# Kernel tuning notes

Hardware: AMD Instinct MI355X
Metric: run time of the kernel (lower is better)

The kernel has to match this reference:

```python
import jax, jax.numpy as jnp
import numpy as np

EPS = 1e-5

def conv_bn(x, w, bn):
    # 1x1 conv (no bias) + BatchNorm2d in eval mode.
    # x: [B,C,H,W], w: [O,C], bn: [4,O] = (gamma, beta, running_mean, running_var)
    y = jnp.einsum('bchw,oc->bohw', x, w)
    g, b, m, v = bn[0], bn[1], bn[2], bn[3]
    s = g * jax.lax.rsqrt(v + EPS)
    return y * s[None, :, None, None] + (b - m * s)[None, :, None, None]

def setup_inputs() -> dict:
    key = jax.random.key(0)
    ks = jax.random.split(key, 10)
    dim, nh_kd, dh = 384, 256, 1024
    return {
        'x':   jax.random.normal(ks[0], (16, dim, 32, 32), dtype=jnp.float32),
        'wq':  jax.random.normal(ks[1], (nh_kd, dim), dtype=jnp.float32) * 0.05,
        'bnq': jax.random.uniform(ks[2], (4, nh_kd), dtype=jnp.float32),
        'wk':  jax.random.normal(ks[3], (nh_kd, dim), dtype=jnp.float32) * 0.05,
        'bnk': jax.random.uniform(ks[4], (4, nh_kd), dtype=jnp.float32),
        'wv':  jax.random.normal(ks[5], (dh, dim), dtype=jnp.float32) * 0.05,
        'bnv': jax.random.uniform(ks[6], (4, dh), dtype=jnp.float32),
        'wp':  jax.random.normal(ks[7], (dim, dh), dtype=jnp.float32) * 0.05,
        'bnp': jax.random.uniform(ks[8], (4, dim), dtype=jnp.float32),
        'num_heads': 8,
    }

def reference(x, wq, bnq, wk, bnk, wv, bnv, wp, bnp, num_heads):
    B, C, H, W = x.shape
    N = H * W
    nh = num_heads
    kd = wq.shape[0] // nh          # key_dim
    d = wv.shape[0] // nh           # attn_ratio * key_dim
    dh = wv.shape[0]
    scale = kd ** (-0.5)

    qq = conv_bn(x, wq, bnq).reshape(B, nh, kd, N).transpose(0, 1, 3, 2)  # [B,nh,N,kd]
    kk = conv_bn(x, wk, bnk).reshape(B, nh, kd, N)                         # [B,nh,kd,N]
    vv = conv_bn(x, wv, bnv).reshape(B, nh, d, N).transpose(0, 1, 3, 2)    # [B,nh,N,d]

    # NOTE: original divides by scale (i.e. multiplies by sqrt(key_dim)); kept faithfully.
    attn = jnp.einsum('bhnk,bhkm->bhnm', qq, kk) / scale
    attn = jax.nn.softmax(attn, axis=-1)
    xx = jnp.einsum('bhnm,bhmd->bhnd', attn, vv)           # [B,nh,N,d]
    xx = xx.transpose(0, 1, 3, 2).reshape(B, dh, H, W)
    return conv_bn(xx, wp, bnp)
```

## Files before the change

### kernel.cpp

```cpp
#include <hip/hip_runtime.h>

typedef _Float16 f16x8 __attribute__((ext_vector_type(8)));
typedef _Float16 f16x4 __attribute__((ext_vector_type(4)));
typedef __fp16 h16x2 __attribute__((ext_vector_type(2)));
typedef float f32x4 __attribute__((ext_vector_type(4)));
typedef float f32x16 __attribute__((ext_vector_type(16)));

#define BN_EPS 1e-5f
#define SQRT32 5.656854249492381f
#define LOG2E  1.4426950408889634f

typedef const __attribute__((address_space(1))) void* gas_p;
typedef __attribute__((address_space(3))) void* las_p;

__global__ __launch_bounds__(256) void prep(
    const float* __restrict__ x,
    const float* __restrict__ wq, const float* __restrict__ wk,
    const float* __restrict__ wv, const float* __restrict__ wp,
    const float* __restrict__ bnq, const float* __restrict__ bnk,
    const float* __restrict__ bnv, const float* __restrict__ bnp,
    _Float16* __restrict__ xT_hi, _Float16* __restrict__ xT_lo,
    _Float16* __restrict__ wqk_h,
    _Float16* __restrict__ wv_h,  _Float16* __restrict__ wp_h,
    float* __restrict__ s_qkv, float* __restrict__ t_qkv,
    float* __restrict__ s_p,   float* __restrict__ t_p)
{
    __shared__ float Tx[64][65];
    const int t = threadIdx.x;
    if (blockIdx.z < 16) {
        const int ct = blockIdx.x, nt = blockIdx.y, b = blockIdx.z;
        const int c0 = ct * 64, n0 = nt * 64;
        {
            int tr = t >> 4, tc = (t & 15) * 4;
            #pragma unroll
            for (int p = 0; p < 4; p++) {
                int r = tr + p * 16;
                float4 v = *(const float4*)(x + ((size_t)(b * 384 + c0 + r)) * 1024 + n0 + tc);
                Tx[r][tc + 0] = v.x; Tx[r][tc + 1] = v.y; Tx[r][tc + 2] = v.z; Tx[r][tc + 3] = v.w;
            }
        }
        __syncthreads();
        {
            int nn = t >> 2, cc = (t & 3) * 16;
            f16x8 h0, h1, l0, l1;
            #pragma unroll
            for (int i = 0; i < 8; i++) {
                float v = Tx[cc + i][nn];
                _Float16 hh = (_Float16)v;
                h0[i] = hh; l0[i] = (_Float16)(v - (float)hh);
            }
            #pragma unroll
            for (int i = 0; i < 8; i++) {
                float v = Tx[cc + 8 + i][nn];
                _Float16 hh = (_Float16)v;
                h1[i] = hh; l1[i] = (_Float16)(v - (float)hh);
            }
            size_t o = ((size_t)(b * 1024 + n0 + nn)) * 384 + c0 + cc;
            *(f16x8*)(xT_hi + o) = h0; *(f16x8*)(xT_hi + o + 8) = h1;
            *(f16x8*)(xT_lo + o) = l0; *(f16x8*)(xT_lo + o + 8) = l1;
        }
    } else {
        const int NQK = 512 * 384, NV = 1024 * 384, NP = 384 * 1024;
        int tid = (blockIdx.y * 6 + blockIdx.x) * 256 + t;
        for (int i = tid; i < NQK + NV + NP; i += 24576) {
            if (i < NQK) {
                int o = i / 384, c = i - o * 384;
                float v = (o < 256) ? wq[o * 384 + c] : wk[(o - 256) * 384 + c];
                wqk_h[i] = (_Float16)v;
            } else if (i < NQK + NV) {
                wv_h[i - NQK] = (_Float16)wv[i - NQK];
            } else {
                wp_h[i - NQK - NV] = (_Float16)wp[i - NQK - NV];
            }
        }
        if (tid < 1536) {
            int i = tid;
            float g, be, m, v;
            if (i < 256)      { int o = i;       g = bnq[o]; be = bnq[256 + o];  m = bnq[512 + o];  v = bnq[768 + o]; }
            else if (i < 512) { int o = i - 256; g = bnk[o]; be = bnk[256 + o];  m = bnk[512 + o];  v = bnk[768 + o]; }
            else              { int o = i - 512; g = bnv[o]; be = bnv[1024 + o]; m = bnv[2048 + o]; v = bnv[3072 + o]; }
            float s = g * rsqrtf(v + BN_EPS);
            float tt = be - m * s;
            if (i < 256) { s *= SQRT32 * LOG2E; tt *= SQRT32 * LOG2E; }
            s_qkv[i] = s; t_qkv[i] = tt;
        } else if (tid < 1536 + 384) {
            int o = tid - 1536;
            float g = bnp[o], be = bnp[384 + o], m = bnp[768 + o], v = bnp[1152 + o];
            float s = g * rsqrtf(v + BN_EPS);
            s_p[o] = s; t_p[o] = be - m * s;
        }
    }
}

__global__ __launch_bounds__(256, 2) void gemm_qkv(
    const _Float16* __restrict__ wqk_h,
    const _Float16* __restrict__ wv_h,
    const _Float16* __restrict__ xT_hi, const _Float16* __restrict__ xT_lo,
    const float* __restrict__ S, const float* __restrict__ T,
    _Float16* __restrict__ qT_h,
    _Float16* __restrict__ kT_h, _Float16* __restrict__ kT_l,
    _Float16* __restrict__ vbuf)
{
    __shared__ __align__(16) _Float16 As_h[128 * 64];
    __shared__ __align__(16) _Float16 Bs_h[128 * 64];
    __shared__ __align__(16) _Float16 Bs_l[128 * 64];
    const int t = threadIdx.x, lane = t & 63, w = t >> 6;
    const int wr = w >> 1, wc = w & 1, l16 = lane & 15, lq = lane >> 4;
    const int bx = blockIdx.x, n0 = blockIdx.y * 128, b = blockIdx.z;
    const bool isv = bx >= 4;
    const int o0 = isv ? (bx - 4) * 128 : bx * 128;
    const _Float16* __restrict__ Ah = isv ? wv_h : wqk_h;

    f32x4 acc[4][4] = {};

    for (int kb = 0; kb < 384; kb += 64) {
        __syncthreads();
        #pragma unroll
        for (int p = 0; p < 4; p++) {
            int g = t + p * 256, row = g >> 3, s = g & 7;
            int col = ((s ^ (row & 7)) * 8);
            __builtin_amdgcn_global_load_lds(
                (gas_p)(const void*)(Ah + (size_t)(o0 + row) * 384 + kb + col),
                (las_p)(void*)&As_h[(p * 256 + w * 64) * 8], 16, 0, 0);
        }
        #pragma unroll
        for (int p = 0; p < 4; p++) {
            int g = t + p * 256, row = g >> 3, s = g & 7;
            int col = ((s ^ (row & 7)) * 8);
            __builtin_amdgcn_global_load_lds(
                (gas_p)(const void*)(xT_hi + ((size_t)(b * 1024) + n0 + row) * 384 + kb + col),
                (las_p)(void*)&Bs_h[(p * 256 + w * 64) * 8], 16, 0, 0);
        }
        if (!isv) {
            #pragma unroll
            for (int p = 0; p < 4; p++) {
                int g = t + p * 256, row = g >> 3, s = g & 7;
                int col = ((s ^ (row & 7)) * 8);
                __builtin_amdgcn_global_load_lds(
                    (gas_p)(const void*)(xT_lo + ((size_t)(b * 1024) + n0 + row) * 384 + kb + col),
                    (las_p)(void*)&Bs_l[(p * 256 + w * 64) * 8], 16, 0, 0);
            }
        }
        __syncthreads();

        if (!isv) {
            #pragma unroll
            for (int kk = 0; kk < 2; kk++) {
                const int sl = ((kk * 4 + lq) ^ (l16 & 7)) * 8;
                f16x8 awh[4], bxh[4], bxl[4];
                #pragma unroll
                for (int i = 0; i < 4; i++)
                    awh[i] = *(const f16x8*)(&As_h[(wr * 64 + i * 16 + l16) * 64 + sl]);
                #pragma unroll
                for (int j = 0; j < 4; j++) {
                    int row = wc * 64 + j * 16 + l16;
                    bxh[j] = *(const f16x8*)(&Bs_h[row * 64 + sl]);
                    bxl[j] = *(const f16x8*)(&Bs_l[row * 64 + sl]);
                }
                #pragma unroll
                for (int i = 0; i < 4; i++)
                    #pragma unroll
                    for (int j = 0; j < 4; j++) {
                        acc[i][j] = __builtin_amdgcn_mfma_f32_16x16x32_f16(awh[i], bxh[j], acc[i][j], 0, 0, 0);
                        acc[i][j] = __builtin_amdgcn_mfma_f32_16x16x32_f16(awh[i], bxl[j], acc[i][j], 0, 0, 0);
                    }
            }
        } else {
            #pragma unroll
            for (int kk = 0; kk < 2; kk++) {
                const int sl = ((kk * 4 + lq) ^ (l16 & 7)) * 8;
                f16x8 axh[4], bwv[4];
                #pragma unroll
                for (int i = 0; i < 4; i++)
                    axh[i] = *(const f16x8*)(&Bs_h[(wr * 64 + i * 16 + l16) * 64 + sl]);
                #pragma unroll
                for (int j = 0; j < 4; j++)
                    bwv[j] = *(const f16x8*)(&As_h[(wc * 64 + j * 16 + l16) * 64 + sl]);
                #pragma unroll
                for (int i = 0; i < 4; i++)
                    #pragma unroll
                    for (int j = 0; j < 4; j++)
                        acc[i][j] = __builtin_amdgcn_mfma_f32_16x16x32_f16(axh[i], bwv[j], acc[i][j], 0, 0, 0);
            }
        }
    }

    if (!isv) {
        #pragma unroll
        for (int i = 0; i < 4; i++) {
            int ob = o0 + wr * 64 + i * 16 + lq * 4;
            float4 sc4 = *(const float4*)(S + ob);
            float4 sh4 = *(const float4*)(T + ob);
            #pragma unroll
            for (int j = 0; j < 4; j++) {
                int n = n0 + wc * 64 + j * 16 + l16;
                f16x4 hv, lv;
                #pragma unroll
                for (int r = 0; r < 4; r++) {
                    float v = acc[i][j][r] * ((const float*)&sc4)[r] + ((const float*)&sh4)[r];
                    _Float16 hh = (_Float16)v;
                    hv[r] = hh; lv[r] = (_Float16)(v - (float)hh);
                }
                if (ob < 256) {
                    size_t idx = (((size_t)(b * 8) + (ob >> 5)) * 1024 + n) * 32 + (ob & 31);
                    *(f16x4*)(qT_h + idx) = hv;
                } else {
                    int oo = ob - 256;
                    int hd = oo >> 5, c = oo & 31;
                    int f = ((n >> 5) & 1) * 2 + (c >> 4);
                    size_t idx = ((((size_t)(b * 8 + hd) * 16 + (n >> 6)) * 4 + f) * 64
                                  + ((c >> 3) & 1) * 32 + (n & 31)) * 8 + (c & 7);
                    *(f16x4*)(kT_h + idx) = hv;
                    *(f16x4*)(kT_l + idx) = lv;
                }
            }
        }
    } else {
        #pragma unroll
        for (int i = 0; i < 4; i++) {
            int epb = i * 16 + (lq & 1) * 8 + (lq >> 1) * 4;
            int nhi = n0 + wr * 64;
            #pragma unroll
            for (int j = 0; j < 4; j++) {
                int o = o0 + wc * 64 + j * 16 + l16;
                float sc = S[512 + o], sh = T[512 + o];
                f16x4 vv;
                #pragma unroll
                for (int r = 0; r < 4; r++)
                    vv[r] = (_Float16)(acc[i][j][r] * sc + sh);
                *(f16x4*)(vbuf + ((size_t)(b * 1024) + o) * 1024 + nhi + epb) = vv;
            }
        }
    }
}

__device__ __forceinline__ f32x16 qk4(f16x8 kh0, f16x8 kl0, f16x8 kh1, f16x8 kl1,
                                      f16x8 qh0, f16x8 qh1) {
    f32x16 c = {};
    c = __builtin_amdgcn_mfma_f32_32x32x16_f16(kh0, qh0, c, 0, 0, 0);
    c = __builtin_amdgcn_mfma_f32_32x32x16_f16(kl0, qh0, c, 0, 0, 0);
    c = __builtin_amdgcn_mfma_f32_32x32x16_f16(kh1, qh1, c, 0, 0, 0);
    c = __builtin_amdgcn_mfma_f32_32x32x16_f16(kl1, qh1, c, 0, 0, 0);
    return c;
}

__global__ __launch_bounds__(256, 2) void attn(
    const _Float16* __restrict__ qT_h,
    const _Float16* __restrict__ kT_h, const _Float16* __restrict__ kT_l,
    const _Float16* __restrict__ vbuf,
    _Float16* __restrict__ xxT_h)
{
    __shared__ __align__(16) _Float16 Vs[3][128 * 64];
    __shared__ __align__(16) _Float16 Ksh[2][2048];
    __shared__ __align__(16) _Float16 Ksl[2][2048];
    const int t = threadIdx.x, lane = t & 63, w = t >> 6;
    const int L = lane & 31, hl = lane >> 5;
    const int bh = blockIdx.x, qt = blockIdx.y;
    const int b = bh >> 3, h = bh & 7;
    const size_t vbase = ((size_t)(b * 1024) + h * 128) * 1024;

    f16x8 bq_h[2];
    {
        int q = qt * 128 + w * 32 + L;
        #pragma unroll
        for (int kh = 0; kh < 2; kh++) {
            size_t base = ((size_t)(bh * 1024) + q) * 32 + kh * 16 + hl * 8;
            bq_h[kh] = *(const f16x8*)(qT_h + base);
        }
    }

    f32x16 o_acc[4] = {};
    float m_st = -INFINITY, l_st = 0.f;
    f16x8 pf[4];

    #define DMA_TILE(vb, kb, kt_)                                                  \
        {                                                                          \
            size_t ktb = (size_t)(bh * 16 + (kt_)) * 2048 + (size_t)t * 8;         \
            __builtin_amdgcn_global_load_lds((gas_p)(const void*)(kT_h + ktb),     \
                                             (las_p)(void*)&Ksh[kb][w * 512], 16, 0, 0); \
            __builtin_amdgcn_global_load_lds((gas_p)(const void*)(kT_l + ktb),     \
                                             (las_p)(void*)&Ksl[kb][w * 512], 16, 0, 0); \
            _Pragma("unroll")                                                      \
            for (int p = 0; p < 4; p++) {                                          \
                int g2 = t + p * 256;                                              \
                int d = g2 >> 3;                                                   \
                int kcg = (g2 & 7) ^ (d & 7);                                      \
                const _Float16* src = vbuf + vbase + (size_t)d * 1024              \
                                      + (kt_) * 64 + kcg * 8;                      \
                _Float16* dst = &Vs[vb][(p * 256 + w * 64) * 8];                   \
                __builtin_amdgcn_global_load_lds((gas_p)(const void*)src,          \
                                                 (las_p)(void*)dst, 16, 0, 0);     \
            }                                                                      \
        }

    DMA_TILE(0, 0, 0)
    __syncthreads();

    for (int kt = 0; kt < 16; kt++) {
        const int kcur = kt & 1;
        const int vprv = (kt + 2) % 3;

        if (kt < 15) DMA_TILE((kt + 1) % 3, kcur ^ 1, kt + 1)

        const _Float16* khp = &Ksh[kcur][lane * 8];
        const _Float16* klp = &Ksl[kcur][lane * 8];
        f16x8 K0h = *(const f16x8*)(khp);
        f16x8 K1h = *(const f16x8*)(khp + 512);
        f16x8 K2h = *(const f16x8*)(khp + 1024);
        f16x8 K3h = *(const f16x8*)(khp + 1536);
        f16x8 K0l = *(const f16x8*)(klp);
        f16x8 K1l = *(const f16x8*)(klp + 512);
        f16x8 K2l = *(const f16x8*)(klp + 1024);
        f16x8 K3l = *(const f16x8*)(klp + 1536);

        __builtin_amdgcn_s_setprio(1);
        f32x16 c0 = qk4(K0h, K0l, K1h, K1l, bq_h[0], bq_h[1]);
        f32x16 c1 = qk4(K2h, K2l, K3h, K3l, bq_h[0], bq_h[1]);
        __builtin_amdgcn_s_setprio(0);

        if (kt) {
            __builtin_amdgcn_s_setprio(1);
            #pragma unroll
            for (int s = 0; s < 4; s++) {
                int cp = (2 * s + hl) ^ (L & 7);
                #pragma unroll
                for (int dt = 0; dt < 4; dt++) {
                    f16x8 avp = *(const f16x8*)(&Vs[vprv][(dt * 32 + L) * 64 + cp * 8]);
                    o_acc[dt] = __builtin_amdgcn_mfma_f32_32x32x16_f16(avp, pf[s], o_acc[dt], 0, 0, 0);
                }
            }
            __builtin_amdgcn_s_setprio(0);
        }

        #define EL(e) ((e) < 16 ? c0[e] : c1[(e) - 16])
        float t1[11];
        #pragma unroll
        for (int g = 0; g < 10; g++)
            t1[g] = fmaxf(fmaxf(EL(3 * g), EL(3 * g + 1)), EL(3 * g + 2));
        t1[10] = fmaxf(EL(30), EL(31));
        #undef EL
        float t2a = fmaxf(fmaxf(t1[0], t1[1]), t1[2]);
        float t2b = fmaxf(fmaxf(t1[3], t1[4]), t1[5]);
        float t2c = fmaxf(fmaxf(t1[6], t1[7]), t1[8]);
        float t2d = fmaxf(t1[9], t1[10]);
        float mx0 = fmaxf(fmaxf(t2a, t2b), fmaxf(t2c, t2d));
        float mx = fmaxf(mx0, __shfl_xor(mx0, 32, 64));

        if (__any(mx > m_st + 8.f)) {
            float mnew = fmaxf(m_st, mx);
            float a = exp2f(m_st - mnew);
            l_st *= a;
            #pragma unroll
            for (int dt = 0; dt < 4; dt++)
                #pragma unroll
                for (int i = 0; i < 16; i++) o_acc[dt][i] *= a;
            m_st = mnew;
        }

        float rs = 0.f;
        #pragma unroll
        for (int s = 0; s < 4; s++) {
            float pv[8];
            #pragma unroll
            for (int j = 0; j < 8; j++) {
                float cv = (s < 2) ? c0[(s & 1) * 8 + j] : c1[(s & 1) * 8 + j];
                pv[j] = exp2f(cv - m_st);
            }
            rs += ((pv[0] + pv[1]) + (pv[2] + pv[3])) + ((pv[4] + pv[5]) + (pv[6] + pv[7]));
            union { f16x8 v; h16x2 hh[4]; } u;
            #pragma unroll
            for (int j = 0; j < 4; j++)
                u.hh[j] = __builtin_amdgcn_cvt_pkrtz(pv[2 * j], pv[2 * j + 1]);
            pf[s] = u.v;
        }
        l_st += rs;

        if (kt < 15) __syncthreads();
    }
    #undef DMA_TILE

    {
        __builtin_amdgcn_s_setprio(1);
        #pragma unroll
        for (int s = 0; s < 4; s++) {
            int cp = (2 * s + hl) ^ (L & 7);
            #pragma unroll
            for (int dt = 0; dt < 4; dt++) {
                f16x8 avp = *(const f16x8*)(&Vs[0][(dt * 32 + L) * 64 + cp * 8]);
                o_acc[dt] = __builtin_amdgcn_mfma_f32_32x32x16_f16(avp, pf[s], o_acc[dt], 0, 0, 0);
            }
        }
        __builtin_amdgcn_s_setprio(0);
    }

    l_st += __shfl_xor(l_st, 32, 64);

    {
        float rl = 1.f / l_st;
        int q = qt * 128 + w * 32 + L;
        #pragma unroll
        for (int dt = 0; dt < 4; dt++) {
            #pragma unroll
            for (int gg = 0; gg < 4; gg++) {
                f16x4 hv;
                #pragma unroll
                for (int rr = 0; rr < 4; rr++)
                    hv[rr] = (_Float16)(o_acc[dt][gg * 4 + rr] * rl);
                size_t o = ((size_t)(b * 1024) + q) * 1024 + h * 128 + dt * 32 + gg * 8 + hl * 4;
                *(f16x4*)(xxT_h + o) = hv;
            }
        }
    }
}

__global__ __launch_bounds__(256, 2) void gemm_out(
    const _Float16* __restrict__ wp_h,
    const _Float16* __restrict__ xxT_h,
    const float* __restrict__ S, const float* __restrict__ T,
    float* __restrict__ out)
{
    __shared__ __align__(16) _Float16 As[128 * 64];
    __shared__ __align__(16) _Float16 Bh[64 * 64];
    const int t = threadIdx.x, lane = t & 63, w = t >> 6;
    const int wr = w >> 1, wc = w & 1, l16 = lane & 15, lq = lane >> 4;
    const int o0 = blockIdx.x * 128, n0 = blockIdx.y * 64, b = blockIdx.z;

    f32x4 acc[2][4] = {};

    for (int kb = 0; kb < 1024; kb += 64) {
        __syncthreads();
        #pragma unroll
        for (int p = 0; p < 4; p++) {
            int g = t + p * 256, row = g >> 3, s = g & 7;
            int col = ((s ^ (row & 7)) * 8);
            __builtin_amdgcn_global_load_lds(
                (gas_p)(const void*)(wp_h + (size_t)(o0 + row) * 1024 + kb + col),
                (las_p)(void*)&As[(p * 256 + w * 64) * 8], 16, 0, 0);
        }
        #pragma unroll
        for (int p = 0; p < 2; p++) {
            int g = t + p * 256, row = g >> 3, s = g & 7;
            int col = ((s ^ (row & 7)) * 8);
            size_t src = ((size_t)(b * 1024) + n0 + row) * 1024 + kb + col;
            __builtin_amdgcn_global_load_lds(
                (gas_p)(const void*)(xxT_h + src),
                (las_p)(void*)&Bh[(p * 256 + w * 64) * 8], 16, 0, 0);
        }
        __syncthreads();

        #pragma unroll
        for (int kk = 0; kk < 2; kk++) {
            const int sl = ((kk * 4 + lq) ^ (l16 & 7)) * 8;
            f16x8 axh[2], bw[4];
            #pragma unroll
            for (int i = 0; i < 2; i++)
                axh[i] = *(const f16x8*)(&Bh[(wc * 32 + i * 16 + l16) * 64 + sl]);
            #pragma unroll
            for (int j = 0; j < 4; j++)
                bw[j] = *(const f16x8*)(&As[(wr * 64 + j * 16 + l16) * 64 + sl]);
            #pragma unroll
            for (int i = 0; i < 2; i++)
                #pragma unroll
                for (int j = 0; j < 4; j++)
                    acc[i][j] = __builtin_amdgcn_mfma_f32_16x16x32_f16(axh[i], bw[j], acc[i][j], 0, 0, 0);
        }
    }

    #pragma unroll
    for (int i = 0; i < 2; i++) {
        int nb = n0 + wc * 32 + i * 16 + lq * 4;
        #pragma unroll
        for (int j = 0; j < 4; j++) {
            int o = o0 + wr * 64 + j * 16 + l16;
            float sc = S[o], sh = T[o];
            float4 vv;
            vv.x = acc[i][j][0] * sc + sh;
            vv.y = acc[i][j][1] * sc + sh;
            vv.z = acc[i][j][2] * sc + sh;
            vv.w = acc[i][j][3] * sc + sh;
            *(float4*)(out + ((size_t)(b * 384) + o) * 1024 + nb) = vv;
        }
    }
}


extern "C" void kernel_launch(void* const* d_in, const int* in_sizes, int n_in,
                              void* d_out, int out_size, void* d_ws, size_t ws_size,
                              hipStream_t stream) {
    const float* x   = (const float*)d_in[0];
    const float* wq  = (const float*)d_in[1];
    const float* bnq = (const float*)d_in[2];
    const float* wk  = (const float*)d_in[3];
    const float* bnk = (const float*)d_in[4];
    const float* wv  = (const float*)d_in[5];
    const float* bnv = (const float*)d_in[6];
    const float* wp  = (const float*)d_in[7];
    const float* bnp = (const float*)d_in[8];
    float* out = (float*)d_out;
    (void)in_sizes; (void)n_in; (void)out_size; (void)ws_size;

    char* ws = (char*)d_ws;
    size_t off = 0;
    auto alloc = [&](size_t bytes) {
        void* p = ws + off;
        off = (off + bytes + 255) & ~(size_t)255;
        return p;
    };
    _Float16* xT_hi = (_Float16*)alloc((size_t)16 * 1024 * 384 * 2);
    _Float16* xT_lo = (_Float16*)alloc((size_t)16 * 1024 * 384 * 2);
    _Float16* wqk_h = (_Float16*)alloc((size_t)512 * 384 * 2);
    _Float16* wv_h  = (_Float16*)alloc((size_t)1024 * 384 * 2);
    alloc((size_t)8 * 1024 * 1024);
    _Float16* xxT_h = (_Float16*)d_ws;
    _Float16* wp_h  = (_Float16*)alloc((size_t)384 * 1024 * 2);
    float*    s_qkv = (float*)alloc(1536 * 4);
    float*    t_qkv = (float*)alloc(1536 * 4);
    float*    s_p   = (float*)alloc(384 * 4);
    float*    t_p   = (float*)alloc(384 * 4);
    _Float16* qT_h  = (_Float16*)alloc((size_t)16 * 8 * 1024 * 32 * 2);
    _Float16* kT_h  = (_Float16*)alloc((size_t)16 * 8 * 1024 * 32 * 2);
    _Float16* kT_l  = (_Float16*)alloc((size_t)16 * 8 * 1024 * 32 * 2);
    _Float16* vbuf  = (_Float16*)alloc((size_t)16 * 1024 * 1024 * 2);

    prep<<<dim3(6, 16, 17), dim3(256), 0, stream>>>(
        x, wq, wk, wv, wp, bnq, bnk, bnv, bnp,
        xT_hi, xT_lo, wqk_h, wv_h, wp_h, s_qkv, t_qkv, s_p, t_p);

    gemm_qkv<<<dim3(12, 8, 16), dim3(256), 0, stream>>>(
        wqk_h, wv_h, xT_hi, xT_lo, s_qkv, t_qkv,
        qT_h, kT_h, kT_l, vbuf);

    attn<<<dim3(128, 8), dim3(256), 0, stream>>>(qT_h, kT_h, kT_l, vbuf, xxT_h);

    gemm_out<<<dim3(3, 16, 16), dim3(256), 0, stream>>>(wp_h, xxT_h, s_p, t_p, out);
}
```

Baseline: 268.9 us.

## Fold softmax max-subtraction into MFMA accumulator init and row-sum into MFMA

The attention kernel stops subtracting the running max per element before exp2. Instead it seeds the QK MFMA accumulator with a negative running-max vector, so the scores come out already shifted. The softmax row sum is now computed with an extra MFMA against a ones vector, which removes the VALU adds and the cross-half shuffle. The two QK accumulation chains are also interleaved to hide MFMA latency. This trades VALU exp and add work for one extra MFMA per s-step, and changes the numerics, since the row sum now uses fp16-rounded probabilities.

New measurement: 258.5 us. -3.9%, faster.

```diff
diff --git a/kernel.cpp b/kernel.cpp
--- a/kernel.cpp
+++ b/kernel.cpp
@@ -234,16 +234,6 @@
     }
 }
 
-__device__ __forceinline__ f32x16 qk4(f16x8 kh0, f16x8 kl0, f16x8 kh1, f16x8 kl1,
-                                      f16x8 qh0, f16x8 qh1) {
-    f32x16 c = {};
-    c = __builtin_amdgcn_mfma_f32_32x32x16_f16(kh0, qh0, c, 0, 0, 0);
-    c = __builtin_amdgcn_mfma_f32_32x32x16_f16(kl0, qh0, c, 0, 0, 0);
-    c = __builtin_amdgcn_mfma_f32_32x32x16_f16(kh1, qh1, c, 0, 0, 0);
-    c = __builtin_amdgcn_mfma_f32_32x32x16_f16(kl1, qh1, c, 0, 0, 0);
-    return c;
-}
-
 __global__ __launch_bounds__(256, 2) void attn(
     const _Float16* __restrict__ qT_h,
     const _Float16* __restrict__ kT_h, const _Float16* __restrict__ kT_l,
@@ -270,7 +260,11 @@
     }
 
     f32x16 o_acc[4] = {};
-    float m_st = -INFINITY, l_st = 0.f;
+    f32x16 lacc = {};
+    f32x16 mInit = {};
+    f16x8 ones;
+    #pragma unroll
+    for (int i = 0; i < 8; i++) ones[i] = (_Float16)1.0f;
     f16x8 pf[4];
 
     #define DMA_TILE(vb, kb, kt_)                                                  \
@@ -314,8 +308,14 @@
         f16x8 K3l = *(const f16x8*)(klp + 1536);
 
         __builtin_amdgcn_s_setprio(1);
-        f32x16 c0 = qk4(K0h, K0l, K1h, K1l, bq_h[0], bq_h[1]);
-        f32x16 c1 = qk4(K2h, K2l, K3h, K3l, bq_h[0], bq_h[1]);
+        f32x16 c0 = __builtin_amdgcn_mfma_f32_32x32x16_f16(K0h, bq_h[0], mInit, 0, 0, 0);
+        f32x16 c1 = __builtin_amdgcn_mfma_f32_32x32x16_f16(K2h, bq_h[0], mInit, 0, 0, 0);
+        c0 = __builtin_amdgcn_mfma_f32_32x32x16_f16(K0l, bq_h[0], c0, 0, 0, 0);
+        c1 = __builtin_amdgcn_mfma_f32_32x32x16_f16(K2l, bq_h[0], c1, 0, 0, 0);
+        c0 = __builtin_amdgcn_mfma_f32_32x32x16_f16(K1h, bq_h[1], c0, 0, 0, 0);
+        c1 = __builtin_amdgcn_mfma_f32_32x32x16_f16(K3h, bq_h[1], c1, 0, 0, 0);
+        c0 = __builtin_amdgcn_mfma_f32_32x32x16_f16(K1l, bq_h[1], c0, 0, 0, 0);
+        c1 = __builtin_amdgcn_mfma_f32_32x32x16_f16(K3l, bq_h[1], c1, 0, 0, 0);
         __builtin_amdgcn_s_setprio(0);
 
         if (kt) {
@@ -328,6 +328,7 @@
                     f16x8 avp = *(const f16x8*)(&Vs[vprv][(dt * 32 + L) * 64 + cp * 8]);
                     o_acc[dt] = __builtin_amdgcn_mfma_f32_32x32x16_f16(avp, pf[s], o_acc[dt], 0, 0, 0);
                 }
+                lacc = __builtin_amdgcn_mfma_f32_32x32x16_f16(ones, pf[s], lacc, 0, 0, 0);
             }
             __builtin_amdgcn_s_setprio(0);
         }
@@ -346,34 +347,36 @@
         float mx0 = fmaxf(fmaxf(t2a, t2b), fmaxf(t2c, t2d));
         float mx = fmaxf(mx0, __shfl_xor(mx0, 32, 64));
 
-        if (__any(mx > m_st + 8.f)) {
-            float mnew = fmaxf(m_st, mx);
-            float a = exp2f(m_st - mnew);
-            l_st *= a;
+        if (kt == 0) {
+            #pragma unroll
+            for (int i = 0; i < 16; i++) { c0[i] -= mx; c1[i] -= mx; mInit[i] -= mx; }
+        } else if (__any(mx > 8.f)) {
+            float d = fmaxf(mx, 0.f);
+            float a = exp2f(-d);
+            #pragma unroll
+            for (int i = 0; i < 16; i++) lacc[i] *= a;
             #pragma unroll
             for (int dt = 0; dt < 4; dt++)
                 #pragma unroll
                 for (int i = 0; i < 16; i++) o_acc[dt][i] *= a;
-            m_st = mnew;
-        }
-
-        float rs = 0.f;
+            #pragma unroll
+            for (int i = 0; i < 16; i++) { c0[i] -= d; c1[i] -= d; mInit[i] -= d; }
+        }
+
         #pragma unroll
         for (int s = 0; s < 4; s++) {
             float pv[8];
             #pragma unroll
             for (int j = 0; j < 8; j++) {
                 float cv = (s < 2) ? c0[(s & 1) * 8 + j] : c1[(s & 1) * 8 + j];
-                pv[j] = exp2f(cv - m_st);
-            }
-            rs += ((pv[0] + pv[1]) + (pv[2] + pv[3])) + ((pv[4] + pv[5]) + (pv[6] + pv[7]));
+                pv[j] = exp2f(cv);
+            }
             union { f16x8 v; h16x2 hh[4]; } u;
             #pragma unroll
             for (int j = 0; j < 4; j++)
                 u.hh[j] = __builtin_amdgcn_cvt_pkrtz(pv[2 * j], pv[2 * j + 1]);
             pf[s] = u.v;
         }
-        l_st += rs;
 
         if (kt < 15) __syncthreads();
     }
@@ -389,14 +392,13 @@
                 f16x8 avp = *(const f16x8*)(&Vs[0][(dt * 32 + L) * 64 + cp * 8]);
                 o_acc[dt] = __builtin_amdgcn_mfma_f32_32x32x16_f16(avp, pf[s], o_acc[dt], 0, 0, 0);
             }
+            lacc = __builtin_amdgcn_mfma_f32_32x32x16_f16(ones, pf[s], lacc, 0, 0, 0);
         }
         __builtin_amdgcn_s_setprio(0);
     }
 
-    l_st += __shfl_xor(l_st, 32, 64);
-
     {
-        float rl = 1.f / l_st;
+        float rl = 1.f / lacc[0];
         int q = qt * 128 + w * 32 + L;
         #pragma unroll
         for (int dt = 0; dt < 4; dt++) {
```
